# Kernel tuning notes

Measured on AMD Instinct MI355X. Metric: run time of the kernel, lower is better.

The kernel has to match this reference:

```python
import jax, jax.numpy as jnp
import numpy as np

M, D, K = 65536, 64, 4096
BETA = 0.25
INIT_STD = 0.1


def setup_inputs() -> dict:
    key = jax.random.key(0)
    k1, k2, k3 = jax.random.split(key, 3)
    z_e = jax.random.normal(k1, (M, D), dtype=jnp.float32)
    codebook_weight = jax.random.normal(k2, (K, D), dtype=jnp.float32) * INIT_STD
    ema_cluster_size = jax.random.uniform(k3, (K,), dtype=jnp.float32)
    return {"z_e": z_e, "codebook_weight": codebook_weight,
            "ema_cluster_size": ema_cluster_size}


def reference(z_e, codebook_weight, ema_cluster_size):
    # Squared-distance matrix: ||z||^2 + ||e||^2 - 2 z.e   -> (M, K)
    z2 = jnp.sum(z_e * z_e, axis=1, keepdims=True)            # (M, 1)
    e2 = jnp.sum(codebook_weight * codebook_weight, axis=1)[None, :]  # (1, K)
    ze = z_e @ codebook_weight.T                               # (M, K)
    dist = z2 + e2 - 2.0 * ze
    indices = jnp.argmin(dist, axis=1)                         # (M,)
    z_q = codebook_weight[indices]                             # (M, D)

    # use_ema=True path (eval mode: no EMA buffer update)
    commit_loss = jnp.mean((z_e - jax.lax.stop_gradient(z_q)) ** 2)
    vq_loss = BETA * commit_loss

    # Straight-through estimator
    z_q_st = z_e + jax.lax.stop_gradient(z_q - z_e)

    # Perplexity from EMA cluster-size buffer
    probs = ema_cluster_size + 1e-10
    probs = probs / jnp.sum(probs)
    perplexity = jnp.exp(-jnp.sum(probs * jnp.log(probs)))
    perplexity = jax.lax.stop_gradient(perplexity)

    return z_q_st, indices, vq_loss, perplexity, z_q
```

## Files before the change

### kernel.cpp

```cpp
#include <hip/hip_runtime.h>
#include <cmath>

#define M_ROWS  65536
#define D_DIM   64
#define K_CODES 4096

#define OFF_IDX  4194304
#define OFF_SCAL 4259840
#define OFF_ZQ   4259842

#define IMG_OFF   (4u << 20)
#define CANDB_OFF 17039368u

#define CH_BYTES 16384
#define CH_QUADS 1024
#define NCHB_F   32
#define NSPLIT   4
#define NCHB     8

typedef _Float16 f16x8 __attribute__((ext_vector_type(8)));
typedef __attribute__((ext_vector_type(4))) float f32x4;
typedef unsigned long long u64;

__device__ __forceinline__ unsigned short f2h(float f) {
  _Float16 h = (_Float16)f;
  return __builtin_bit_cast(unsigned short, h);
}
__device__ __forceinline__ float h2f(unsigned short u) {
  return (float)__builtin_bit_cast(_Float16, u);
}
__device__ __forceinline__ unsigned int umin_(unsigned int a, unsigned int b) {
  return a < b ? a : b;
}
__device__ __forceinline__ unsigned int med3_u32(unsigned int a, unsigned int b, unsigned int c) {
  unsigned int d;
  asm("v_med3_u32 %0, %1, %2, %3" : "=v"(d) : "v"(a), "v"(b), "v"(c));
  return d;
}

__device__ __forceinline__ void gload_lds16(const void* g, void* l) {
  __builtin_amdgcn_global_load_lds((const __attribute__((address_space(1))) void*)g,
                                   (__attribute__((address_space(3))) void*)l, 16, 0, 0);
}
__device__ __forceinline__ void gload_lds4(const void* g, void* l) {
  __builtin_amdgcn_global_load_lds((const __attribute__((address_space(1))) void*)g,
                                   (__attribute__((address_space(3))) void*)l, 4, 0, 0);
}

__device__ __forceinline__ float exact_dist(const float4* z4, float z2,
                                            const float* __restrict__ cb,
                                            const float* __restrict__ e2, int k) {
  const float4* ev = (const float4*)(cb + (size_t)k * 64);
  float4 a0 = make_float4(0.f, 0.f, 0.f, 0.f);
  float4 a1 = make_float4(0.f, 0.f, 0.f, 0.f);
  float4 a2 = make_float4(0.f, 0.f, 0.f, 0.f);
  float4 a3 = make_float4(0.f, 0.f, 0.f, 0.f);
#pragma unroll
  for (int q = 0; q < 4; ++q) {
    float4 e0 = ev[4 * q + 0], e1 = ev[4 * q + 1], e2v = ev[4 * q + 2], e3 = ev[4 * q + 3];
    a0.x = fmaf(z4[4 * q + 0].x, e0.x, a0.x); a0.y = fmaf(z4[4 * q + 0].y, e0.y, a0.y);
    a0.z = fmaf(z4[4 * q + 0].z, e0.z, a0.z); a0.w = fmaf(z4[4 * q + 0].w, e0.w, a0.w);
    a1.x = fmaf(z4[4 * q + 1].x, e1.x, a1.x); a1.y = fmaf(z4[4 * q + 1].y, e1.y, a1.y);
    a1.z = fmaf(z4[4 * q + 1].z, e1.z, a1.z); a1.w = fmaf(z4[4 * q + 1].w, e1.w, a1.w);
    a2.x = fmaf(z4[4 * q + 2].x, e2v.x, a2.x); a2.y = fmaf(z4[4 * q + 2].y, e2v.y, a2.y);
    a2.z = fmaf(z4[4 * q + 2].z, e2v.z, a2.z); a2.w = fmaf(z4[4 * q + 2].w, e2v.w, a2.w);
    a3.x = fmaf(z4[4 * q + 3].x, e3.x, a3.x); a3.y = fmaf(z4[4 * q + 3].y, e3.y, a3.y);
    a3.z = fmaf(z4[4 * q + 3].z, e3.z, a3.z); a3.w = fmaf(z4[4 * q + 3].w, e3.w, a3.w);
  }
  float d;
  {
#pragma clang fp contract(off)
    float sx = (a0.x + a1.x) + (a2.x + a3.x);
    float sy = (a0.y + a1.y) + (a2.y + a3.y);
    float sz = (a0.z + a1.z) + (a2.z + a3.z);
    float sw = (a0.w + a1.w) + (a2.w + a3.w);
    float dot = (sx + sy) + (sz + sw);
    float tt = z2 + e2[k];
    d = tt - 2.0f * dot;
  }
  return d;
}

__device__ __forceinline__ float exact_z2(const float4* z4) {
#pragma clang fp contract(off)
  float rr[8];
  {
    const float* f = (const float*)&z4[0];
#pragma unroll
    for (int j = 0; j < 8; ++j) rr[j] = f[j] * f[j];
  }
#pragma unroll
  for (int a = 1; a < 8; ++a) {
    const float* f = (const float*)&z4[2 * a];
#pragma unroll
    for (int j = 0; j < 8; ++j) rr[j] = rr[j] + f[j] * f[j];
  }
  return ((rr[0] + rr[1]) + (rr[2] + rr[3])) + ((rr[4] + rr[5]) + (rr[6] + rr[7]));
}

__device__ __forceinline__ unsigned int ford(float f) {
  unsigned int b = __float_as_uint(f);
  return b ^ ((((int)b) >> 31) | 0x80000000u);
}

__global__ void prep_kernel(const float* __restrict__ cb, char* __restrict__ img,
                            float* __restrict__ e2, float* __restrict__ e2b) {
  int t = blockIdx.x * 256 + threadIdx.x;
  {
    int k  = t >> 4;
    int d0 = (t & 15) * 4;
    float4 f = ((const float4*)cb)[t];
    ushort4 hi;
    hi.x = f2h(f.x);
    hi.y = f2h(f.y);
    hi.z = f2h(f.z);
    hi.w = f2h(f.w);
    int c = k >> 7, r = k & 127;
    int g = d0 >> 3;
    int off = ((g + r) & 7) * 16 + (d0 & 7) * 2;
    char* base = img + (size_t)c * CH_BYTES + r * 128;
    *(ushort4*)(base + off) = hi;
  }
  if (t < K_CODES) {
    const float4* row = (const float4*)(cb + (size_t)t * D_DIM);
    float4 q[16];
#pragma unroll
    for (int i = 0; i < 16; ++i) q[i] = row[i];
    float s = exact_z2(q);
    e2[t] = s;
    e2b[t] = s + 32.0f;
  }
}

__global__ __launch_bounds__(512, 4)
void vq_full_kernel(const float* __restrict__ z_e,
                    const char* __restrict__ img,
                    const float* __restrict__ e2b,
                    const float* __restrict__ cb,
                    const float* __restrict__ e2,
                    float* __restrict__ out,
                    double* __restrict__ partials) {
  __shared__ union {
    uint4 q[2][CH_QUADS];
    char raw[2][CH_BYTES];
    unsigned int cand[128 * 33];
  } sm;
  __shared__ float lds_e2[2][128];
  __shared__ int sidx[128];
  __shared__ double red[8];
  const int tid  = threadIdx.x;
  const int wave = tid >> 6, lane = tid & 63;
  const int quad = lane >> 4, c16 = lane & 15;
  const int R0   = blockIdx.x * 128;

  {
    const uint4* src = (const uint4*)img;
    gload_lds16(src + tid, &sm.q[0][tid]);
    gload_lds16(src + tid + 512, &sm.q[0][tid + 512]);
    if (tid < 128) gload_lds4(e2b + tid, &lds_e2[0][tid]);
  }

  f16x8 zh[2];
  {
    int m = R0 + wave * 16 + c16;
#pragma unroll
    for (int s = 0; s < 2; ++s) {
      const float* zp = z_e + (size_t)m * 64 + s * 32 + quad * 8;
      float4 fa = ((const float4*)zp)[0];
      float4 fb = ((const float4*)zp)[1];
      float v[8] = {fa.x, fa.y, fa.z, fa.w, fb.x, fb.y, fb.z, fb.w};
      union { f16x8 v8; unsigned short e[8]; } H;
#pragma unroll
      for (int j = 0; j < 8; ++j) H.e[j] = f2h(-2.0f * v[j]);
      zh[s] = H.v8;
    }
  }

  unsigned int b1[4], b2[4];
#pragma unroll
  for (int r = 0; r < 4; ++r) { b1[r] = 0xFFFFFFFFu; b2[r] = 0xFFFFFFFFu; }

  const int swz0 = ((quad + c16) & 7) * 16;
  const int swz1 = ((quad + 4 + c16) & 7) * 16;

  __syncthreads();

  int cur = 0;
  for (int c = 0; c < NCHB_F; ++c) {
    if (c + 1 < NCHB_F) {
      const int nb = cur ^ 1;
      const uint4* src = (const uint4*)(img + (size_t)(c + 1) * CH_BYTES);
      gload_lds16(src + tid, &sm.q[nb][tid]);
      gload_lds16(src + tid + 512, &sm.q[nb][tid + 512]);
      if (tid < 128) gload_lds4(e2b + (c + 1) * 128 + tid, &lds_e2[nb][tid]);
    }

#pragma unroll 1
    for (int t = 0; t < 8; ++t) {
      const char* hb = sm.raw[cur] + (t * 16 + c16) * 128;
      f16x8 Bh0 = *(const f16x8*)(hb + swz0);
      f16x8 Bh1 = *(const f16x8*)(hb + swz1);
      float e2v = lds_e2[cur][t * 16 + c16];
      unsigned int tid8 = (unsigned int)(c * 8 + t);
      f32x4 cvec = {e2v, e2v, e2v, e2v};

      f32x4 acc;
      acc = __builtin_amdgcn_mfma_f32_16x16x32_f16(zh[0], Bh0, cvec, 0, 0, 0);
      acc = __builtin_amdgcn_mfma_f32_16x16x32_f16(zh[1], Bh1, acc, 0, 0, 0);
#pragma unroll
      for (int r = 0; r < 4; ++r) {
        unsigned int key = (__float_as_uint(acc[r]) & 0xFFFFFF00u) | tid8;
        b2[r] = med3_u32(b1[r], b2[r], key);
        b1[r] = umin_(b1[r], key);
      }
    }
    __syncthreads();
    cur ^= 1;
  }

  {
#pragma unroll
    for (int r = 0; r < 4; ++r) {
      int lr = wave * 16 + quad * 4 + r;
      sm.cand[lr * 33 + c16 * 2 + 0] = b1[r];
      sm.cand[lr * 33 + c16 * 2 + 1] = b2[r];
    }
  }
  __syncthreads();
  if (tid < 128) {
    unsigned int kk[4] = {0xFFFFFFFFu, 0xFFFFFFFFu, 0xFFFFFFFFu, 0xFFFFFFFFu};
    unsigned int vv[4] = {0, 0, 0, 0};
    for (int j = 0; j < 32; ++j) {
      unsigned int key = sm.cand[tid * 33 + j];
      if (key < kk[3]) {
        kk[3] = key;
        vv[3] = (key & 0xFFu) * 16 + (unsigned int)(j >> 1);
        for (int p = 3; p > 0; --p)
          if (kk[p] < kk[p - 1]) {
            unsigned int a = kk[p]; kk[p] = kk[p - 1]; kk[p - 1] = a;
            unsigned int b = vv[p]; vv[p] = vv[p - 1]; vv[p - 1] = b;
          }
      }
    }
    const int row = R0 + tid;
    unsigned int key1 = kk[0] & 0xFFFFFF00u;
    unsigned int key2 = kk[1] & 0xFFFFFF00u;
    int bk;
    if ((key2 - key1) >= 2048u) {
      bk = (int)vv[0];
    } else {
      const float4* zr = (const float4*)(z_e + (size_t)row * 64);
      float4 z4[16];
#pragma unroll
      for (int j = 0; j < 16; ++j) z4[j] = zr[j];
      float z2 = exact_z2(z4);
      float bd = INFINITY;
      bk = K_CODES;
#pragma unroll 1
      for (int ci = 0; ci < 4; ++ci) {
        int k = (int)vv[ci];
        float d = exact_dist(z4, z2, cb, e2, k);
        if (d < bd || (d == bd && k < bk)) { bd = d; bk = k; }
      }
    }
    sidx[tid] = bk;
    out[OFF_IDX + row] = (float)bk;
  }
  __syncthreads();

  double csum = 0.0;
#pragma unroll
  for (int p = 0; p < 4; ++p) {
    const int lr  = p * 32 + (tid >> 4);
    const int m   = R0 + lr;
    const int seg = tid & 15;
    const int k   = sidx[lr];
    float4 q = *(const float4*)(cb + (size_t)k * 64 + seg * 4);
    float4 z = *(const float4*)(z_e + (size_t)m * 64 + seg * 4);
    ((float4*)out)[(size_t)m * 16 + seg] = q;
    float* d1 = out + OFF_ZQ + (size_t)m * 64 + seg * 4;
    ((float2*)d1)[0] = make_float2(q.x, q.y);
    ((float2*)d1)[1] = make_float2(q.z, q.w);
    float dx = z.x - q.x, dy = z.y - q.y, dz = z.z - q.z, dw = z.w - q.w;
    csum += (double)dx * dx + (double)dy * dy + (double)dz * dz + (double)dw * dw;
  }
#pragma unroll
  for (int off = 32; off > 0; off >>= 1) csum += __shfl_down(csum, off);
  if (lane == 0) red[wave] = csum;
  __syncthreads();
  if (tid == 0) {
    double s = 0.0;
#pragma unroll
    for (int w = 0; w < 8; ++w) s += red[w];
    partials[blockIdx.x] = s;
  }
}

__global__ __launch_bounds__(512, 4)
void vq_mfma_kernel(const float* __restrict__ z_e,
                    const char* __restrict__ img,
                    const float* __restrict__ e2b,
                    u64* __restrict__ cand64) {
  __shared__ union {
    uint4 q[2][CH_QUADS];
    char raw[2][CH_BYTES];
    unsigned int cand[256 * 33];
  } sm;
  __shared__ float lds_e2[2][128];
  const int tid  = threadIdx.x;
  const int wave = tid >> 6, lane = tid & 63;
  const int quad = lane >> 4, c16 = lane & 15;
  const int rb   = blockIdx.x >> 2;
  const int sp   = blockIdx.x & 3;
  const int mb   = rb * 256 + wave * 32;

  {
    const uint4* src = (const uint4*)(img + (size_t)(sp * NCHB + 0) * CH_BYTES);
    gload_lds16(src + tid, &sm.q[0][tid]);
    gload_lds16(src + tid + 512, &sm.q[0][tid + 512]);
    if (tid < 128) gload_lds4(e2b + sp * 1024 + 0 * 128 + tid, &lds_e2[0][tid]);
  }

  f16x8 zh[2][2];
#pragma unroll
  for (int mt = 0; mt < 2; ++mt) {
    int m = mb + mt * 16 + c16;
#pragma unroll
    for (int s = 0; s < 2; ++s) {
      const float* zp = z_e + (size_t)m * 64 + s * 32 + quad * 8;
      float4 fa = ((const float4*)zp)[0];
      float4 fb = ((const float4*)zp)[1];
      float v[8] = {fa.x, fa.y, fa.z, fa.w, fb.x, fb.y, fb.z, fb.w};
      union { f16x8 v8; unsigned short e[8]; } H;
#pragma unroll
      for (int j = 0; j < 8; ++j) H.e[j] = f2h(-2.0f * v[j]);
      zh[mt][s] = H.v8;
    }
  }

  unsigned int b1[2][4], b2[2][4];
#pragma unroll
  for (int mt = 0; mt < 2; ++mt)
#pragma unroll
    for (int r = 0; r < 4; ++r) { b1[mt][r] = 0xFFFFFFFFu; b2[mt][r] = 0xFFFFFFFFu; }

  const int swz0 = ((quad + c16) & 7) * 16;
  const int swz1 = ((quad + 4 + c16) & 7) * 16;

  __syncthreads();

  int cur = 0;
  for (int c = 0; c < NCHB; ++c) {
    if (c + 1 < NCHB) {
      const int nb = cur ^ 1;
      const uint4* src = (const uint4*)(img + (size_t)(sp * NCHB + c + 1) * CH_BYTES);
      gload_lds16(src + tid, &sm.q[nb][tid]);
      gload_lds16(src + tid + 512, &sm.q[nb][tid + 512]);
      if (tid < 128) gload_lds4(e2b + sp * 1024 + (c + 1) * 128 + tid, &lds_e2[nb][tid]);
    }

#pragma unroll 1
    for (int t = 0; t < 8; ++t) {
      const char* hb = sm.raw[cur] + (t * 16 + c16) * 128;
      f16x8 Bh0 = *(const f16x8*)(hb + swz0);
      f16x8 Bh1 = *(const f16x8*)(hb + swz1);
      float e2v = lds_e2[cur][t * 16 + c16];
      unsigned int tid8 = (unsigned int)(sp * 64 + c * 8 + t);
      f32x4 cvec = {e2v, e2v, e2v, e2v};

#pragma unroll
      for (int mt = 0; mt < 2; ++mt) {
        f32x4 acc;
        acc = __builtin_amdgcn_mfma_f32_16x16x32_f16(zh[mt][0], Bh0, cvec, 0, 0, 0);
        acc = __builtin_amdgcn_mfma_f32_16x16x32_f16(zh[mt][1], Bh1, acc, 0, 0, 0);
#pragma unroll
        for (int r = 0; r < 4; ++r) {
          unsigned int key = (__float_as_uint(acc[r]) & 0xFFFFFF00u) | tid8;
          b2[mt][r] = med3_u32(b1[mt][r], b2[mt][r], key);
          b1[mt][r] = umin_(b1[mt][r], key);
        }
      }
    }
    __syncthreads();
    cur ^= 1;
  }

  __syncthreads();
  {
#pragma unroll
    for (int mt = 0; mt < 2; ++mt)
#pragma unroll
      for (int r = 0; r < 4; ++r) {
        int lr = wave * 32 + mt * 16 + quad * 4 + r;
        sm.cand[lr * 33 + c16 * 2 + 0] = b1[mt][r];
        sm.cand[lr * 33 + c16 * 2 + 1] = b2[mt][r];
      }
  }
  __syncthreads();
  if (tid < 256) {
    unsigned int kk[4] = {0xFFFFFFFFu, 0xFFFFFFFFu, 0xFFFFFFFFu, 0xFFFFFFFFu};
    unsigned int vv[4] = {0, 0, 0, 0};
    for (int j = 0; j < 32; ++j) {
      unsigned int key = sm.cand[tid * 33 + j];
      if (key < kk[3]) {
        kk[3] = key;
        vv[3] = (key & 0xFFu) * 16 + (unsigned int)(j >> 1);
        for (int p = 3; p > 0; --p)
          if (kk[p] < kk[p - 1]) {
            unsigned int a = kk[p]; kk[p] = kk[p - 1]; kk[p - 1] = a;
            unsigned int b = vv[p]; vv[p] = vv[p - 1]; vv[p - 1] = b;
          }
      }
    }
    int grow = rb * 256 + tid;
#pragma unroll
    for (int i = 0; i < 4; ++i)
      cand64[(size_t)grow * 16 + sp * 4 + i] = ((u64)kk[i] << 32) | (u64)vv[i];
  }
}

__device__ __forceinline__ void pick_scan4(const u64* __restrict__ cand64,
                                           int row, int part, u64& s1, u64& s2) {
  s1 = ~0ull; s2 = ~0ull;
  const u64* cp = cand64 + (size_t)row * 16 + part * 4;
#pragma unroll
  for (int j = 0; j < 4; ++j) {
    u64 v = cp[j];
    if (v < s1) { s2 = s1; s1 = v; }
    else if (v < s2) s2 = v;
  }
#pragma unroll
  for (int m = 1; m <= 2; m <<= 1) {
    u64 o1 = __shfl_xor(s1, m);
    u64 o2 = __shfl_xor(s2, m);
    u64 hi  = s1 > o1 ? s1 : o1;
    u64 lo2 = s2 < o2 ? s2 : o2;
    s1 = s1 < o1 ? s1 : o1;
    s2 = hi < lo2 ? hi : lo2;
  }
}

__device__ __forceinline__ int pick_exact16(const float* __restrict__ z_e,
                                            const float* __restrict__ cb,
                                            const float* __restrict__ e2,
                                            const u64* __restrict__ cand64,
                                            int row, int lane16) {
  const int k = (int)(unsigned int)(cand64[(size_t)row * 16 + lane16] & 0xFFFFFFFFu);
  const float4* zr = (const float4*)(z_e + (size_t)row * 64);
  float4 z4[16];
#pragma unroll
  for (int j = 0; j < 16; ++j) z4[j] = zr[j];
  float z2 = exact_z2(z4);
  float d = exact_dist(z4, z2, cb, e2, k);
  u64 kk = ((u64)ford(d) << 32) | (unsigned int)k;
#pragma unroll
  for (int m = 1; m <= 8; m <<= 1) {
    u64 o = __shfl_xor(kk, m);
    kk = o < kk ? o : kk;
  }
  return (int)(unsigned int)(kk & 0xFFFFFFFFu);
}

__global__ __launch_bounds__(256)
void pick_kernel(const float* __restrict__ z_e, const float* __restrict__ cb,
                 const float* __restrict__ e2, const u64* __restrict__ cand64,
                 float* __restrict__ out) {
  __shared__ int list[64];
  __shared__ int lcnt;
  const int tid = threadIdx.x;
  const int R0  = blockIdx.x * 64;
  if (tid == 0) lcnt = 0;
  __syncthreads();

  {
    const int row = R0 + (tid >> 2);
    u64 s1, s2;
    pick_scan4(cand64, row, tid & 3, s1, s2);
    if ((tid & 3) == 0) {
      unsigned int key1 = (unsigned int)(s1 >> 32) & 0xFFFFFF00u;
      unsigned int key2 = (unsigned int)(s2 >> 32) & 0xFFFFFF00u;
      if ((key2 - key1) >= 2048u) {
        out[OFF_IDX + row] = (float)(unsigned int)(s1 & 0xFFFFFFFFu);
      } else {
        list[atomicAdd(&lcnt, 1)] = row - R0;
      }
    }
  }
  __syncthreads();

  const int n = lcnt;
  const int lane16 = tid & 15;
  for (int g = tid >> 4; g < n; g += 16) {
    const int row = R0 + list[g];
    int bk = pick_exact16(z_e, cb, e2, cand64, row, lane16);
    if (lane16 == 0) out[OFF_IDX + row] = (float)bk;
  }
}

__global__ __launch_bounds__(256)
void zq_kernel(const float* __restrict__ z_e, const float* __restrict__ cb,
               float* __restrict__ out, double* __restrict__ partials) {
  const int tid = threadIdx.x;
  const int t   = blockIdx.x * 256 + tid;
  const int m   = t >> 4, seg = t & 15;

  int k = (int)out[OFF_IDX + m];
  float4 q = *(const float4*)(cb + (size_t)k * 64 + seg * 4);
  float4 z = *(const float4*)(z_e + (size_t)m * 64 + seg * 4);

  ((float4*)out)[(size_t)m * 16 + seg] = q;
  float* d1 = out + OFF_ZQ + (size_t)m * 64 + seg * 4;
  ((float2*)d1)[0] = make_float2(q.x, q.y);
  ((float2*)d1)[1] = make_float2(q.z, q.w);

  float dx = z.x - q.x, dy = z.y - q.y, dz = z.z - q.z, dw = z.w - q.w;
  double csum = (double)dx * dx + (double)dy * dy + (double)dz * dz + (double)dw * dw;
#pragma unroll
  for (int off = 32; off > 0; off >>= 1) csum += __shfl_down(csum, off);
  if ((tid & 63) == 0) partials[blockIdx.x * 4 + (tid >> 6)] = csum;
}

__global__ void finalize_kernel(const float* __restrict__ ema,
                                const double* __restrict__ partials, int n,
                                float* __restrict__ out) {
  __shared__ double red[1024];
  const int t = threadIdx.x;

  double cs = 0.0;
  for (int i = t; i < n; i += 1024) cs += partials[i];
  red[t] = cs;
  __syncthreads();
  for (int off = 512; off > 0; off >>= 1) {
    if (t < off) red[t] += red[t + off];
    __syncthreads();
  }
  double commit = red[0];
  __syncthreads();

  double s = 0.0;
  for (int i = t; i < K_CODES; i += 1024) s += (double)(ema[i] + 1e-10f);
  red[t] = s;
  __syncthreads();
  for (int off = 512; off > 0; off >>= 1) {
    if (t < off) red[t] += red[t + off];
    __syncthreads();
  }
  double S = red[0];
  __syncthreads();

  double h = 0.0;
  for (int i = t; i < K_CODES; i += 1024) {
    float p = (float)((ema[i] + 1e-10f) / (float)S);
    h += (double)(p * logf(p));
  }
  red[t] = h;
  __syncthreads();
  for (int off = 512; off > 0; off >>= 1) {
    if (t < off) red[t] += red[t + off];
    __syncthreads();
  }

  if (t == 0) {
    out[OFF_SCAL]     = 0.25f * (float)(commit / (double)((size_t)M_ROWS * (size_t)D_DIM));
    out[OFF_SCAL + 1] = expf((float)(-red[0]));
  }
}

extern "C" void kernel_launch(void* const* d_in, const int* in_sizes, int n_in,
                              void* d_out, int out_size, void* d_ws, size_t ws_size,
                              hipStream_t stream) {
  (void)in_sizes; (void)n_in; (void)out_size;
  const float* z_e = (const float*)d_in[0];
  const float* cb  = (const float*)d_in[1];
  const float* ema = (const float*)d_in[2];
  float* out = (float*)d_out;

  float*  e2       = (float*)d_ws;
  float*  e2b      = (float*)((char*)d_ws + 16384);
  double* partials = (double*)((char*)d_ws + 32768);
  const size_t fused_need = 163840 + 524288;

  if (ws_size >= fused_need) {
    char* img = (char*)d_ws + 163840;
    prep_kernel<<<(K_CODES * D_DIM / 4) / 256, 256, 0, stream>>>(cb, img, e2, e2b);
    vq_full_kernel<<<M_ROWS / 128, 512, 0, stream>>>(z_e, img, e2b, cb, e2, out, partials);
    finalize_kernel<<<1, 1024, 0, stream>>>(ema, partials, M_ROWS / 128, out);
  } else {
    char* img = (char*)d_out + IMG_OFF;
    u64* cand64 = (u64*)((char*)d_out + CANDB_OFF);
    prep_kernel<<<(K_CODES * D_DIM / 4) / 256, 256, 0, stream>>>(cb, img, e2, e2b);
    vq_mfma_kernel<<<(M_ROWS / 256) * NSPLIT, 512, 0, stream>>>(z_e, img, e2b, cand64);
    pick_kernel<<<M_ROWS / 64, 256, 0, stream>>>(z_e, cb, e2, cand64, out);
    zq_kernel<<<M_ROWS * 16 / 256, 256, 0, stream>>>(z_e, cb, out, partials);
    finalize_kernel<<<1, 1024, 0, stream>>>(ema, partials, 16384, out);
  }
}
```

Measured before the change: 147.7 us.

## Double codebook stage size and fold finalize into last-block reduction

The fused VQ kernel now streams the codebook in 16 phases of 256 codes (32 KB per buffer) instead of 32 chunks of 128, and fully unrolls the inner tile loop, halving the number of barriers and prefetch rounds. The separate finalize launch is removed: each block atomically publishes its partial and bumps a counter, and the last block computes the commit loss and perplexity. This trades one kernel launch and per-chunk sync overhead for doubled LDS use, which may lower occupancy, plus a serial tail in the last block.

Measured after the change: 157.2 us. 1.06x slower.

```diff
diff --git a/kernel.cpp b/kernel.cpp
--- a/kernel.cpp
+++ b/kernel.cpp
@@ -13,10 +13,11 @@
 #define CANDB_OFF 17039368u
 
 #define CH_BYTES 16384
-#define CH_QUADS 1024
-#define NCHB_F   32
+#define NPH_F    16
+#define PH_QUADS 2048
 #define NSPLIT   4
 #define NCHB     8
+#define CH_QUADS 1024
 
 typedef _Float16 f16x8 __attribute__((ext_vector_type(8)));
 typedef __attribute__((ext_vector_type(4))) float f32x4;
@@ -104,8 +105,10 @@
 }
 
 __global__ void prep_kernel(const float* __restrict__ cb, char* __restrict__ img,
-                            float* __restrict__ e2, float* __restrict__ e2b) {
+                            float* __restrict__ e2, float* __restrict__ e2b,
+                            unsigned int* __restrict__ ctr) {
   int t = blockIdx.x * 256 + threadIdx.x;
+  if (t == 0 && ctr) *ctr = 0u;
   {
     int k  = t >> 4;
     int d0 = (t & 15) * 4;
@@ -138,16 +141,20 @@
                     const float* __restrict__ e2b,
                     const float* __restrict__ cb,
                     const float* __restrict__ e2,
+                    const float* __restrict__ ema,
                     float* __restrict__ out,
-                    double* __restrict__ partials) {
+                    double* __restrict__ partials,
+                    unsigned int* __restrict__ ctr) {
   __shared__ union {
-    uint4 q[2][CH_QUADS];
-    char raw[2][CH_BYTES];
+    uint4 q[2][PH_QUADS];
+    char raw[2][2 * CH_BYTES];
     unsigned int cand[128 * 33];
   } sm;
-  __shared__ float lds_e2[2][128];
+  __shared__ float lds_e2[2][256];
   __shared__ int sidx[128];
   __shared__ double red[8];
+  __shared__ double bc[2];
+  __shared__ int is_last;
   const int tid  = threadIdx.x;
   const int wave = tid >> 6, lane = tid & 63;
   const int quad = lane >> 4, c16 = lane & 15;
@@ -155,9 +162,9 @@
 
   {
     const uint4* src = (const uint4*)img;
-    gload_lds16(src + tid, &sm.q[0][tid]);
-    gload_lds16(src + tid + 512, &sm.q[0][tid + 512]);
-    if (tid < 128) gload_lds4(e2b + tid, &lds_e2[0][tid]);
+#pragma unroll
+    for (int i = 0; i < 4; ++i) gload_lds16(src + tid + i * 512, &sm.q[0][tid + i * 512]);
+    if (tid < 256) gload_lds4(e2b + tid, &lds_e2[0][tid]);
   }
 
   f16x8 zh[2];
@@ -186,22 +193,22 @@
   __syncthreads();
 
   int cur = 0;
-  for (int c = 0; c < NCHB_F; ++c) {
-    if (c + 1 < NCHB_F) {
+  for (int p = 0; p < NPH_F; ++p) {
+    if (p + 1 < NPH_F) {
       const int nb = cur ^ 1;
-      const uint4* src = (const uint4*)(img + (size_t)(c + 1) * CH_BYTES);
-      gload_lds16(src + tid, &sm.q[nb][tid]);
-      gload_lds16(src + tid + 512, &sm.q[nb][tid + 512]);
-      if (tid < 128) gload_lds4(e2b + (c + 1) * 128 + tid, &lds_e2[nb][tid]);
-    }
-
-#pragma unroll 1
-    for (int t = 0; t < 8; ++t) {
-      const char* hb = sm.raw[cur] + (t * 16 + c16) * 128;
-      f16x8 Bh0 = *(const f16x8*)(hb + swz0);
-      f16x8 Bh1 = *(const f16x8*)(hb + swz1);
+      const uint4* src = (const uint4*)(img + (size_t)(p + 1) * 2 * CH_BYTES);
+#pragma unroll
+      for (int i = 0; i < 4; ++i) gload_lds16(src + tid + i * 512, &sm.q[nb][tid + i * 512]);
+      if (tid < 256) gload_lds4(e2b + (p + 1) * 256 + tid, &lds_e2[nb][tid]);
+    }
+
+    const char* hb0 = sm.raw[cur] + c16 * 128;
+#pragma unroll
+    for (int t = 0; t < 16; ++t) {
+      f16x8 Bh0 = *(const f16x8*)(hb0 + t * 2048 + swz0);
+      f16x8 Bh1 = *(const f16x8*)(hb0 + t * 2048 + swz1);
       float e2v = lds_e2[cur][t * 16 + c16];
-      unsigned int tid8 = (unsigned int)(c * 8 + t);
+      unsigned int tid8 = (unsigned int)(p * 16 + t);
       f32x4 cvec = {e2v, e2v, e2v, e2v};
 
       f32x4 acc;
@@ -292,7 +299,60 @@
     double s = 0.0;
 #pragma unroll
     for (int w = 0; w < 8; ++w) s += red[w];
-    partials[blockIdx.x] = s;
+    atomicExch((unsigned long long*)&partials[blockIdx.x], __double_as_longlong(s));
+    __threadfence();
+    unsigned int old = atomicAdd(ctr, 1u);
+    is_last = (old == gridDim.x - 1) ? 1 : 0;
+  }
+  __syncthreads();
+
+  if (is_last) {
+    __threadfence();
+    double v = __longlong_as_double(
+        atomicAdd((unsigned long long*)&partials[tid], 0ull));
+#pragma unroll
+    for (int off = 32; off > 0; off >>= 1) v += __shfl_down(v, off);
+    if (lane == 0) red[wave] = v;
+    __syncthreads();
+    if (tid == 0) {
+      double commit = 0.0;
+#pragma unroll
+      for (int w = 0; w < 8; ++w) commit += red[w];
+      bc[0] = commit;
+    }
+    __syncthreads();
+
+    double s = 0.0;
+    for (int i = tid; i < K_CODES; i += 512) s += (double)(ema[i] + 1e-10f);
+#pragma unroll
+    for (int off = 32; off > 0; off >>= 1) s += __shfl_down(s, off);
+    if (lane == 0) red[wave] = s;
+    __syncthreads();
+    if (tid == 0) {
+      double S = 0.0;
+#pragma unroll
+      for (int w = 0; w < 8; ++w) S += red[w];
+      bc[1] = S;
+    }
+    __syncthreads();
+    const double S = bc[1];
+
+    double h = 0.0;
+    for (int i = tid; i < K_CODES; i += 512) {
+      float p = (float)((ema[i] + 1e-10f) / (float)S);
+      h += (double)(p * logf(p));
+    }
+#pragma unroll
+    for (int off = 32; off > 0; off >>= 1) h += __shfl_down(h, off);
+    if (lane == 0) red[wave] = h;
+    __syncthreads();
+    if (tid == 0) {
+      double hh = 0.0;
+#pragma unroll
+      for (int w = 0; w < 8; ++w) hh += red[w];
+      out[OFF_SCAL]     = 0.25f * (float)(bc[0] / (double)((size_t)M_ROWS * (size_t)D_DIM));
+      out[OFF_SCAL + 1] = expf((float)(-hh));
+    }
   }
 }
 
@@ -578,17 +638,18 @@
   float*  e2       = (float*)d_ws;
   float*  e2b      = (float*)((char*)d_ws + 16384);
   double* partials = (double*)((char*)d_ws + 32768);
+  unsigned int* ctr = (unsigned int*)((char*)d_ws + 32768 + 8192);
   const size_t fused_need = 163840 + 524288;
 
   if (ws_size >= fused_need) {
     char* img = (char*)d_ws + 163840;
-    prep_kernel<<<(K_CODES * D_DIM / 4) / 256, 256, 0, stream>>>(cb, img, e2, e2b);
-    vq_full_kernel<<<M_ROWS / 128, 512, 0, stream>>>(z_e, img, e2b, cb, e2, out, partials);
-    finalize_kernel<<<1, 1024, 0, stream>>>(ema, partials, M_ROWS / 128, out);
+    prep_kernel<<<(K_CODES * D_DIM / 4) / 256, 256, 0, stream>>>(cb, img, e2, e2b, ctr);
+    vq_full_kernel<<<M_ROWS / 128, 512, 0, stream>>>(z_e, img, e2b, cb, e2, ema,
+                                                     out, partials, ctr);
   } else {
     char* img = (char*)d_out + IMG_OFF;
     u64* cand64 = (u64*)((char*)d_out + CANDB_OFF);
-    prep_kernel<<<(K_CODES * D_DIM / 4) / 256, 256, 0, stream>>>(cb, img, e2, e2b);
+    prep_kernel<<<(K_CODES * D_DIM / 4) / 256, 256, 0, stream>>>(cb, img, e2, e2b, nullptr);
     vq_mfma_kernel<<<(M_ROWS / 256) * NSPLIT, 512, 0, stream>>>(z_e, img, e2b, cand64);
     pick_kernel<<<M_ROWS / 64, 256, 0, stream>>>(z_e, cb, e2, cand64, out);
     zq_kernel<<<M_ROWS * 16 / 256, 256, 0, stream>>>(z_e, cb, out, partials);
```
